# Kernel tuning notes

Measured on AMD Instinct MI355X. Metric: run time of the kernel, lower is better.

Reference implementation:

```python
import jax, jax.numpy as jnp
import numpy as np

N_NODES, N_LINKS, N_PATHS = 512, 4096, 20000
D = 128        # node_state_dim == path_state_dim
HEADS = 24
R = 256        # readout units
T_STEPS = 3    # config['t']
MAX_LEN = 8


def _gru(x, h, W, U, b):
    # Keras GRUCell (reset_after=True), gate order [z, r, h]
    xg = x @ W + b[0]
    hg = h @ U + b[1]
    xz, xr, xh = jnp.split(xg, 3, axis=-1)
    hz, hr, hh = jnp.split(hg, 3, axis=-1)
    z = jax.nn.sigmoid(xz + hz)
    r = jax.nn.sigmoid(xr + hr)
    hc = jnp.tanh(xh + r * hh)
    return z * h + (1.0 - z) * hc


def _masked_gru(x_seq, mask, h0, W, U, b, reverse):
    # x_seq [P,T,D], mask [P,T]; Keras masked RNN semantics:
    # state copies through masked steps, output copies previous output (init 0)
    if reverse:
        x_seq = x_seq[:, ::-1]
        mask = mask[:, ::-1]
    def step(carry, inp):
        h, o = carry
        x_t, m_t = inp
        h_new = _gru(x_t, h, W, U, b)
        m = m_t[:, None]
        h = jnp.where(m, h_new, h)
        o = jnp.where(m, h_new, o)
        return (h, o), o
    (hT, _), outs = jax.lax.scan(step, (h0, jnp.zeros_like(h0)),
                                 (x_seq.transpose(1, 0, 2), mask.T))
    outs = outs.transpose(1, 0, 2)
    if reverse:
        outs = outs[:, ::-1]
    return outs, hT


def _gat(x, adj, W, a_self, a_neigh, bias):
    # spektral-style dense GraphAttention, concat_heads=False (mean over heads)
    xp = jnp.einsum('nf,fhc->nhc', x, W)                 # [N,H,C]
    e_s = jnp.einsum('nhc,hc->nh', xp, a_self)
    e_n = jnp.einsum('nhc,hc->nh', xp, a_neigh)
    logits = e_s.T[:, :, None] + e_n.T[:, None, :]       # [H,N,N]
    logits = jax.nn.leaky_relu(logits, 0.2)
    logits = jnp.where(adj[None] == 0.0, -1e9, logits)
    attn = jax.nn.softmax(logits, axis=-1)
    return jnp.einsum('hij,jhc->ihc', attn, xp).mean(axis=1) + bias


def setup_inputs() -> dict:
    rng = np.random.default_rng(0)
    lens = rng.integers(4, MAX_LEN + 1, size=N_PATHS)
    paths = np.repeat(np.arange(N_PATHS, dtype=np.int32), lens)
    seqs = np.concatenate([np.arange(l, dtype=np.int32) for l in lens])
    nodes = rng.integers(0, N_NODES, size=paths.shape[0]).astype(np.int32)
    adj_idx = rng.choice(N_NODES * N_NODES, size=N_LINKS, replace=False).astype(np.int32)

    key = jax.random.key(0)
    ks = iter(jax.random.split(key, 40))
    nrm = lambda *s: jax.random.normal(next(ks), s, dtype=jnp.float32) * 0.05
    unif = lambda *s: jax.random.uniform(next(ks), s, dtype=jnp.float32)
    return {
        'ToS': unif(N_PATHS), 'bandwith': unif(N_PATHS),
        'q_policy': jnp.asarray(rng.integers(0, 3, N_NODES), jnp.float32),
        'w1': unif(N_NODES), 'w2': unif(N_NODES), 'w3': unif(N_NODES),
        'queue_size': unif(N_NODES, 3), 'link_capacity': unif(N_LINKS),
        'gat_W': nrm(D, HEADS, D), 'gat_as': nrm(HEADS, D), 'gat_an': nrm(HEADS, D),
        'gat_b': jnp.zeros((D,), jnp.float32),
        'Wp': nrm(D, 3 * D), 'Up': nrm(D, 3 * D), 'bp': jnp.zeros((2, 3 * D), jnp.float32),
        'Wb': nrm(D, 3 * D), 'Ub': nrm(D, 3 * D), 'bb': jnp.zeros((2, 3 * D), jnp.float32),
        'Wn': nrm(D, 3 * D), 'Un': nrm(D, 3 * D), 'bn': jnp.zeros((2, 3 * D), jnp.float32),
        'rW1': nrm(D, R), 'rb1': jnp.zeros((R,), jnp.float32),
        'rW2': nrm(R, R), 'rb2': jnp.zeros((R,), jnp.float32),
        'rW3': nrm(R, 1), 'rb3': jnp.zeros((1,), jnp.float32),
        'paths': jnp.asarray(paths), 'seqs': jnp.asarray(seqs),
        'nodes': jnp.asarray(nodes), 'adj_idx': jnp.asarray(adj_idx),
    }


def reference(ToS, bandwith, q_policy, w1, w2, w3, queue_size, link_capacity,
              gat_W, gat_as, gat_an, gat_b, Wp, Up, bp, Wb, Ub, bb, Wn, Un, bn,
              rW1, rb1, rW2, rb2, rW3, rb3, paths, seqs, nodes, adj_idx):
    node_state = jnp.concatenate([q_policy[:, None], w1[:, None], w2[:, None],
                                  w3[:, None], queue_size,
                                  jnp.zeros((N_NODES, D - 7), jnp.float32)], axis=1)
    path_state = jnp.concatenate([bandwith[:, None], ToS[:, None],
                                  jnp.zeros((N_PATHS, D - 2), jnp.float32)], axis=1)
    adj = jnp.zeros(N_NODES * N_NODES, jnp.float32).at[adj_idx].set(link_capacity)
    adj = adj.reshape(N_NODES, N_NODES)
    adj = adj / jnp.sqrt(jnp.sum(adj * adj))  # tf.linalg.normalize (global L2)

    lens = jax.ops.segment_sum(jnp.ones_like(paths), paths, num_segments=N_PATHS)
    mask = jnp.arange(MAX_LEN)[None, :] < lens[:, None]  # [P,T]

    for _ in range(T_STEPS):
        node_state = _gat(node_state, adj, gat_W, gat_as, gat_an, gat_b)
        h_tild = node_state[nodes]  # [S,D]
        node_inputs = jnp.zeros((N_PATHS, MAX_LEN, D), jnp.float32).at[paths, seqs].set(h_tild)
        out_f, h_f = _masked_gru(node_inputs, mask, path_state, Wp, Up, bp, False)
        out_b, _ = _masked_gru(node_inputs, mask, path_state, Wb, Ub, bb, True)
        outputs = out_f + out_b  # Bidirectional merge_mode='sum'
        path_state = h_f
        m2 = outputs[paths, seqs]
        m2 = jax.ops.segment_sum(m2, nodes, num_segments=N_NODES)
        node_state = _gru(m2, node_state, Wn, Un, bn)

    h = jax.nn.selu(path_state @ rW1 + rb1)
    h = jax.nn.relu(h @ rW2 + rb2)
    return h @ rW3 + rb3
```

## Files before the change

kernel.cpp:

```cpp
#include <hip/hip_runtime.h>
#include <math.h>

#define NN 512
#define NP 20000
#define DD 128
#define NH 24
#define G3 384
#define NHD 3072

typedef __attribute__((ext_vector_type(8))) short bf8_t;
typedef __attribute__((ext_vector_type(4))) float f4_t;
typedef unsigned short ushort_t;

__device__ __forceinline__ float sigf(float x){
  return __builtin_amdgcn_rcpf(1.f + __expf(-x));
}
__device__ __forceinline__ float tanh_fast(float x){
  float ax = fabsf(x);
  float e = __expf(-2.f*ax);
  float t = (1.f - e) * __builtin_amdgcn_rcpf(1.f + e);
  return copysignf(t, x);
}
__device__ __forceinline__ unsigned short f2bf(float f){
  unsigned int u = __float_as_uint(f);
  unsigned int r = (u + 0x7fffu + ((u>>16)&1u)) >> 16;
  return (unsigned short)r;
}
__device__ __forceinline__ float bf2f(unsigned short h){
  return __uint_as_float(((unsigned int)h)<<16);
}

__global__ void k_init_ns(float* ns, const float* qp, const float* w1, const float* w2,
                          const float* w3, const float* qs){
  int n = blockIdx.x, c = threadIdx.x;
  float v = 0.f;
  if (c==0) v=qp[n]; else if (c==1) v=w1[n]; else if (c==2) v=w2[n]; else if (c==3) v=w3[n];
  else if (c<7) v=qs[n*3 + (c-4)];
  ns[n*DD+c]=v;
}

__global__ void k_init_ps(float* ps, const float* bw, const float* tos){
  int i = blockIdx.x*256 + threadIdx.x;
  if (i >= NP*DD) return;
  int p = i>>7, c = i&127;
  float v=0.f; if(c==0) v=bw[p]; else if(c==1) v=tos[p];
  ps[i]=v;
}

__global__ void k_adj(unsigned int* adjb, const int* idx, const float* lc){
  int l = blockIdx.x*256+threadIdx.x; if(l>=4096) return;
  if (lc[l]!=0.f){
    int a = idx[l]; int i = a>>9, j = a&511;
    atomicOr(&adjb[i*16 + (j>>5)], 1u<<(j&31));
  }
}

__global__ void k_meta(const int* paths, const int* seqs, int* start, int* lens, int E){
  int e = blockIdx.x*256+threadIdx.x; if(e>=E) return;
  int p=paths[e], s=seqs[e];
  if (s==0) start[p]=e;
  if (e==E-1 || paths[e+1]!=p) lens[p]=s+1;
}

__global__ void k_lcount(const int* __restrict__ lens, int* lcnt){
  int p = blockIdx.x*256+threadIdx.x; if(p>=NP) return;
  atomicAdd(&lcnt[lens[p]],1);
}
__global__ void k_lscan(const int* __restrict__ lcnt, int* loff, int* lcur){
  if (threadIdx.x==0){
    int acc=0;
    for (int L=15; L>=0; --L){ loff[L]=acc; lcur[L]=acc; acc+=lcnt[L]; }
  }
}
__global__ void k_lfill(const int* __restrict__ lens, int* lcur, int* perm){
  int p = blockIdx.x*256+threadIdx.x; if(p>=NP) return;
  int pos = atomicAdd(&lcur[lens[p]],1);
  perm[pos]=p;
}

__global__ void k_wsplit(const float* __restrict__ W, ushort_t* __restrict__ Wh,
                         ushort_t* __restrict__ Wl, int shift, int ncols, int total){
  int i = blockIdx.x*256 + threadIdx.x;
  if (i >= total) return;
  int col = i >> shift, k = i & ((1<<shift)-1);
  float v = W[(size_t)k*ncols + col];
  ushort_t h = f2bf(v);
  Wh[i] = h; Wl[i] = f2bf(v - bf2f(h));
}

__global__ void k_wsplit6(
    const float* S0,const float* S1,const float* S2,const float* S3,const float* S4,const float* S5,
    ushort_t* H0, ushort_t* L0, ushort_t* H1, ushort_t* L1, ushort_t* H2, ushort_t* L2,
    ushort_t* H3, ushort_t* L3, ushort_t* H4, ushort_t* L4, ushort_t* H5, ushort_t* L5){
  int i = blockIdx.x*256 + threadIdx.x;
  if (i >= 6*G3*DD) return;
  int m = i/(G3*DD), r = i - m*(G3*DD);
  const float* S = m==0?S0:m==1?S1:m==2?S2:m==3?S3:m==4?S4:S5;
  ushort_t* Hh = m==0?H0:m==1?H1:m==2?H2:m==3?H3:m==4?H4:H5;
  ushort_t* Ll = m==0?L0:m==1?L1:m==2?L2:m==3?L3:m==4?L4:L5;
  int col = r>>7, k = r&127;
  float v = S[(size_t)k*G3 + col];
  ushort_t h = f2bf(v);
  Hh[r] = h; Ll[r] = f2bf(v - bf2f(h));
}

__global__ void k_gbw(const float* __restrict__ gb,
                      const float* __restrict__ Wp, const float* __restrict__ Wb,
                      const float* __restrict__ Un,
                      const float* __restrict__ bp, const float* __restrict__ bb,
                      float* bxgF, float* bxgB, float* gbUn){
  int m = blockIdx.x; int j = threadIdx.x;
  const float* W = m==0?Wp:(m==1?Wb:Un);
  float a = m==0?bp[j]:(m==1?bb[j]:0.f);
  for (int k=0;k<128;k++) a += gb[k]*W[(size_t)k*G3+j];
  (m==0?bxgF:(m==1?bxgB:gbUn))[j]=a;
}

__global__ __launch_bounds__(512) void k_xp2(const float* __restrict__ ns,
                      const ushort_t* __restrict__ gwh, const ushort_t* __restrict__ gwl,
                      const float* __restrict__ as_, const float* __restrict__ an_,
                      float* __restrict__ xp, float* __restrict__ es, float* __restrict__ en){
  __shared__ __align__(16) ushort_t XsH[32][136], XsL[32][136];
  __shared__ float ered[8][32][2];
  int r0 = blockIdx.x*32, c0 = blockIdx.y*256;
  int tid = threadIdx.x;
  int w = tid>>6, l = tid&63, lr = l&15, lg = l>>4;
  for (int idx=tid; idx<32*128; idx+=512){
    int pp=idx>>7, kk=idx&127;
    float v = ns[(size_t)(r0+pp)*DD+kk];
    ushort_t hi=f2bf(v); XsH[pp][kk]=hi; XsL[pp][kk]=f2bf(v-bf2f(hi));
  }
  __syncthreads();
  int col0 = c0 + w*32 + lr, col1 = col0 + 16;
  f4_t a00=(f4_t)(0.f), a01=(f4_t)(0.f), a10=(f4_t)(0.f), a11=(f4_t)(0.f);
  #pragma unroll
  for (int kt=0; kt<4; kt++){
    int kof = kt*32 + lg*8;
    const bf8_t Ah0 = *(const bf8_t*)&XsH[lr][kof];
    const bf8_t Al0 = *(const bf8_t*)&XsL[lr][kof];
    const bf8_t Ah1 = *(const bf8_t*)&XsH[16+lr][kof];
    const bf8_t Al1 = *(const bf8_t*)&XsL[16+lr][kof];
    const bf8_t B0h = *(const bf8_t*)(gwh + (size_t)col0*128 + kof);
    const bf8_t B0l = *(const bf8_t*)(gwl + (size_t)col0*128 + kof);
    const bf8_t B1h = *(const bf8_t*)(gwh + (size_t)col1*128 + kof);
    const bf8_t B1l = *(const bf8_t*)(gwl + (size_t)col1*128 + kof);
    a00 = __builtin_amdgcn_mfma_f32_16x16x32_bf16(Ah0,B0h,a00,0,0,0);
    a00 = __builtin_amdgcn_mfma_f32_16x16x32_bf16(Al0,B0h,a00,0,0,0);
    a00 = __builtin_amdgcn_mfma_f32_16x16x32_bf16(Ah0,B0l,a00,0,0,0);
    a01 = __builtin_amdgcn_mfma_f32_16x16x32_bf16(Ah0,B1h,a01,0,0,0);
    a01 = __builtin_amdgcn_mfma_f32_16x16x32_bf16(Al0,B1h,a01,0,0,0);
    a01 = __builtin_amdgcn_mfma_f32_16x16x32_bf16(Ah0,B1l,a01,0,0,0);
    a10 = __builtin_amdgcn_mfma_f32_16x16x32_bf16(Ah1,B0h,a10,0,0,0);
    a10 = __builtin_amdgcn_mfma_f32_16x16x32_bf16(Al1,B0h,a10,0,0,0);
    a10 = __builtin_amdgcn_mfma_f32_16x16x32_bf16(Ah1,B0l,a10,0,0,0);
    a11 = __builtin_amdgcn_mfma_f32_16x16x32_bf16(Ah1,B1h,a11,0,0,0);
    a11 = __builtin_amdgcn_mfma_f32_16x16x32_bf16(Al1,B1h,a11,0,0,0);
    a11 = __builtin_amdgcn_mfma_f32_16x16x32_bf16(Ah1,B1l,a11,0,0,0);
  }
  #pragma unroll
  for (int q=0;q<4;q++){
    int row0 = lg*4+q, row1 = 16+lg*4+q;
    xp[(size_t)(r0+row0)*NHD + col0] = a00[q];
    xp[(size_t)(r0+row0)*NHD + col1] = a01[q];
    xp[(size_t)(r0+row1)*NHD + col0] = a10[q];
    xp[(size_t)(r0+row1)*NHD + col1] = a11[q];
  }
  {
    int hw = blockIdx.y*2 + (w>>2);
    int cc0 = (w*32 + lr)&127, cc1 = (w*32 + 16 + lr)&127;
    float as0 = as_[hw*DD+cc0], as1 = as_[hw*DD+cc1];
    float an0 = an_[hw*DD+cc0], an1 = an_[hw*DD+cc1];
    #pragma unroll
    for (int q=0;q<4;q++){
      float s0 = a00[q]*as0 + a01[q]*as1;
      float n0 = a00[q]*an0 + a01[q]*an1;
      float s1 = a10[q]*as0 + a11[q]*as1;
      float n1 = a10[q]*an0 + a11[q]*an1;
      #pragma unroll
      for (int o=1;o<16;o<<=1){
        s0 += __shfl_xor(s0,o); n0 += __shfl_xor(n0,o);
        s1 += __shfl_xor(s1,o); n1 += __shfl_xor(n1,o);
      }
      if (lr==0){
        ered[w][lg*4+q][0]=s0;    ered[w][lg*4+q][1]=n0;
        ered[w][16+lg*4+q][0]=s1; ered[w][16+lg*4+q][1]=n1;
      }
    }
  }
  __syncthreads();
  if (tid < 128){
    int row = tid&31, hh = (tid>>5)&1, which = tid>>6;
    float v = ered[hh*4+0][row][which] + ered[hh*4+1][row][which]
            + ered[hh*4+2][row][which] + ered[hh*4+3][row][which];
    float* dst = which? en : es;
    dst[(size_t)(r0+row)*NH + blockIdx.y*2 + hh] = v;
  }
}

__global__ __launch_bounds__(256) void k_attn(const float* __restrict__ xp,
                      const float* __restrict__ es, const float* __restrict__ en,
                      const unsigned int* __restrict__ adjb, float* __restrict__ gout){
  __shared__ float lg[32][513];
  __shared__ float mxs[32], isms[32];
  int h = blockIdx.x, it = blockIdx.y; int i0 = it*32; int tid = threadIdx.x;
  for (int idx=tid; idx<32*512; idx+=256){
    int ii = idx>>9, j = idx&511;
    float l = es[(i0+ii)*NH+h] + en[j*NH+h];
    l = (l>=0.f)? l : 0.2f*l;
    unsigned int m = adjb[(i0+ii)*16 + (j>>5)];
    if (!((m>>(j&31))&1u)) l = -1000000000.0f;
    lg[ii][j] = l;
  }
  __syncthreads();
  {
    int t8 = tid&7, ii = tid>>3;
    float m = -INFINITY;
    for (int j=t8;j<512;j+=8) m = fmaxf(m, lg[ii][j]);
    for (int o=4;o>0;o>>=1) m = fmaxf(m, __shfl_xor(m, o));
    float s=0.f;
    for (int j=t8;j<512;j+=8) s += __expf(lg[ii][j]-m);
    for (int o=4;o>0;o>>=1) s += __shfl_xor(s,o);
    if (t8==0){ mxs[ii]=m; isms[ii]=__builtin_amdgcn_rcpf(s); }
  }
  __syncthreads();
  for (int idx=tid; idx<32*512; idx+=256){
    int ii = idx>>9, j = idx&511;
    lg[ii][j] = __expf(lg[ii][j]-mxs[ii])*isms[ii];
  }
  __syncthreads();
  int cq = tid&31, iq = tid>>5; int c = cq*4;
  float4 acc0=make_float4(0,0,0,0), acc1=acc0, acc2=acc0, acc3=acc0;
  for (int j=0;j<512;j++){
    const float4 xv = *(const float4*)(xp + ((size_t)j*NH + h)*DD + c);
    float p0 = lg[iq*4+0][j], p1 = lg[iq*4+1][j], p2 = lg[iq*4+2][j], p3 = lg[iq*4+3][j];
    acc0.x+=p0*xv.x; acc0.y+=p0*xv.y; acc0.z+=p0*xv.z; acc0.w+=p0*xv.w;
    acc1.x+=p1*xv.x; acc1.y+=p1*xv.y; acc1.z+=p1*xv.z; acc1.w+=p1*xv.w;
    acc2.x+=p2*xv.x; acc2.y+=p2*xv.y; acc2.z+=p2*xv.z; acc2.w+=p2*xv.w;
    acc3.x+=p3*xv.x; acc3.y+=p3*xv.y; acc3.z+=p3*xv.z; acc3.w+=p3*xv.w;
  }
  const float inv = 1.f/24.f;
  float* o0 = gout + (size_t)(i0+iq*4+0)*DD + c;
  float* o1 = gout + (size_t)(i0+iq*4+1)*DD + c;
  float* o2 = gout + (size_t)(i0+iq*4+2)*DD + c;
  float* o3 = gout + (size_t)(i0+iq*4+3)*DD + c;
  atomicAdd(o0+0,acc0.x*inv); atomicAdd(o0+1,acc0.y*inv); atomicAdd(o0+2,acc0.z*inv); atomicAdd(o0+3,acc0.w*inv);
  atomicAdd(o1+0,acc1.x*inv); atomicAdd(o1+1,acc1.y*inv); atomicAdd(o1+2,acc1.z*inv); atomicAdd(o1+3,acc1.w*inv);
  atomicAdd(o2+0,acc2.x*inv); atomicAdd(o2+1,acc2.y*inv); atomicAdd(o2+2,acc2.z*inv); atomicAdd(o2+3,acc2.w*inv);
  atomicAdd(o3+0,acc3.x*inv); atomicAdd(o3+1,acc3.y*inv); atomicAdd(o3+2,acc3.z*inv); atomicAdd(o3+3,acc3.w*inv);
}

__global__ __launch_bounds__(512) void k_xg3(const float* __restrict__ gout,
      const ushort_t* __restrict__ WpH, const ushort_t* __restrict__ WpL,
      const ushort_t* __restrict__ WbH, const ushort_t* __restrict__ WbL,
      const float* __restrict__ bxgF, const float* __restrict__ bxgB,
      float* __restrict__ xgF, float* __restrict__ xgB){
  __shared__ __align__(16) ushort_t XsH[32][136], XsL[32][136];
  int r0 = blockIdx.x*32;
  int mat = blockIdx.y/3, cg = blockIdx.y%3;
  const ushort_t* Wh = mat? WbH : WpH;
  const ushort_t* Wl = mat? WbL : WpL;
  const float* b0 = mat? bxgB : bxgF;
  float* out = mat? xgB : xgF;
  int tid = threadIdx.x;
  int w = tid>>6, l = tid&63, lr = l&15, lg = l>>4;
  for (int idx=tid; idx<32*128; idx+=512){
    int pp=idx>>7, kk=idx&127;
    float v = gout[(size_t)(r0+pp)*DD+kk];
    ushort_t hi=f2bf(v); XsH[pp][kk]=hi; XsL[pp][kk]=f2bf(v-bf2f(hi));
  }
  __syncthreads();
  int col = cg*128 + w*16 + lr;
  f4_t a0=(f4_t)(0.f), a1=(f4_t)(0.f);
  #pragma unroll
  for (int kt=0; kt<4; kt++){
    int kof = kt*32 + lg*8;
    const bf8_t Ah0 = *(const bf8_t*)&XsH[lr][kof];
    const bf8_t Al0 = *(const bf8_t*)&XsL[lr][kof];
    const bf8_t Ah1 = *(const bf8_t*)&XsH[16+lr][kof];
    const bf8_t Al1 = *(const bf8_t*)&XsL[16+lr][kof];
    const bf8_t Bh = *(const bf8_t*)(Wh + (size_t)col*128 + kof);
    const bf8_t Bl = *(const bf8_t*)(Wl + (size_t)col*128 + kof);
    a0 = __builtin_amdgcn_mfma_f32_16x16x32_bf16(Ah0,Bh,a0,0,0,0);
    a0 = __builtin_amdgcn_mfma_f32_16x16x32_bf16(Al0,Bh,a0,0,0,0);
    a0 = __builtin_amdgcn_mfma_f32_16x16x32_bf16(Ah0,Bl,a0,0,0,0);
    a1 = __builtin_amdgcn_mfma_f32_16x16x32_bf16(Ah1,Bh,a1,0,0,0);
    a1 = __builtin_amdgcn_mfma_f32_16x16x32_bf16(Al1,Bh,a1,0,0,0);
    a1 = __builtin_amdgcn_mfma_f32_16x16x32_bf16(Ah1,Bl,a1,0,0,0);
  }
  float bb0 = b0[col];
  #pragma unroll
  for (int q=0;q<4;q++){
    out[(size_t)(r0+lg*4+q)*G3 + col]    = a0[q] + bb0;
    out[(size_t)(r0+16+lg*4+q)*G3 + col] = a1[q] + bb0;
  }
}

__global__ __launch_bounds__(512) void k_gru2(
    const float* __restrict__ ps_in, float* __restrict__ ps_out,
    const float* __restrict__ xgF, const float* __restrict__ xgB,
    const ushort_t* __restrict__ UthF, const ushort_t* __restrict__ UtlF,
    const ushort_t* __restrict__ UthB, const ushort_t* __restrict__ UtlB,
    const float* __restrict__ b1F, const float* __restrict__ b1B,
    const int* __restrict__ start, const int* __restrict__ lens,
    const int* __restrict__ nodes, const int* __restrict__ perm,
    float* __restrict__ m2)
{
  __shared__ __align__(16) ushort_t HsH[2][32][136];
  __shared__ __align__(16) ushort_t HsL[2][32][136];
  __shared__ int Ls[32], Ss[32], Pid[32];
  __shared__ int nid_l[32][8];

  int dir = blockIdx.x & 1, pblk = blockIdx.x >> 1;
  const bool rev = (dir==1);
  const float* xg = rev ? xgB : xgF;
  const ushort_t* Uth = rev ? UthB : UthF;
  const ushort_t* Utl = rev ? UtlB : UtlF;
  const float* b1 = rev ? b1B : b1F;
  float* psn = rev ? (float*)0 : ps_out;

  int pb = pblk*32;
  int tid = threadIdx.x;
  int w = tid>>6, l = tid&63;
  int lr = l&15, lg = l>>4;
  int c = w*16 + lr;

  if (tid<32){ int pid = perm[pb+tid]; Pid[tid]=pid; Ls[tid]=lens[pid]; Ss[tid]=start[pid]; }
  __syncthreads();
  for (int idx=tid; idx<32*128; idx+=512){
    int pp=idx>>7, kk=idx&127;
    float v = ps_in[(size_t)Pid[pp]*DD+kk];
    ushort_t hi = f2bf(v);
    HsH[0][pp][kk]=hi; HsL[0][pp][kk]=f2bf(v - bf2f(hi));
  }
  if (tid<256){
    int p=tid>>3, s=tid&7; int L=Ls[p];
    int nid = 0;
    if (s<L){ int pos = rev ? (L-1-s) : s; nid = nodes[Ss[p]+pos]; }
    nid_l[p][s]=nid;
  }
  __syncthreads();

  int Lmax = Ls[0];
  int Lv[8];
  #pragma unroll
  for (int i=0;i<8;i++){ int p=(i>>2)*16 + lg*4 + (i&3); Lv[i]=Ls[p]; }
  float b1z = b1[c], b1r = b1[128+c], b1h = b1[256+c];

  int cur = 0;
  for (int s=0;s<Lmax;s++){
    int nxt = cur^1;
    bool act[8]; int niv[8]; float xzv[8], xrv[8], xhv[8];
    #pragma unroll
    for (int i=0;i<8;i++){
      int p=(i>>2)*16 + lg*4 + (i&3);
      act[i] = (s < Lv[i]);
      int nid = nid_l[p][s];
      niv[i] = nid;
      const float* xr = xg + (size_t)nid*G3;
      xzv[i]=xr[c]; xrv[i]=xr[128+c]; xhv[i]=xr[256+c];
    }
    f4_t accz0=(f4_t)(0.f), accz1=(f4_t)(0.f);
    f4_t accr0=(f4_t)(0.f), accr1=(f4_t)(0.f);
    f4_t acch0=(f4_t)(0.f), acch1=(f4_t)(0.f);
    #pragma unroll
    for (int kt=0; kt<4; kt++){
      int kof = kt*32 + lg*8;
      const bf8_t Ahi0 = *(const bf8_t*)&HsH[cur][lr][kof];
      const bf8_t Alo0 = *(const bf8_t*)&HsL[cur][lr][kof];
      const bf8_t Ahi1 = *(const bf8_t*)&HsH[cur][16+lr][kof];
      const bf8_t Alo1 = *(const bf8_t*)&HsL[cur][16+lr][kof];
      const bf8_t Bhz = *(const bf8_t*)(Uth + ((size_t)(      c))*128 + kof);
      const bf8_t Blz = *(const bf8_t*)(Utl + ((size_t)(      c))*128 + kof);
      const bf8_t Bhr = *(const bf8_t*)(Uth + ((size_t)(128 + c))*128 + kof);
      const bf8_t Blr = *(const bf8_t*)(Utl + ((size_t)(128 + c))*128 + kof);
      const bf8_t Bhh = *(const bf8_t*)(Uth + ((size_t)(256 + c))*128 + kof);
      const bf8_t Blh = *(const bf8_t*)(Utl + ((size_t)(256 + c))*128 + kof);
      accz0 = __builtin_amdgcn_mfma_f32_16x16x32_bf16(Ahi0, Bhz, accz0, 0,0,0);
      accz0 = __builtin_amdgcn_mfma_f32_16x16x32_bf16(Alo0, Bhz, accz0, 0,0,0);
      accz0 = __builtin_amdgcn_mfma_f32_16x16x32_bf16(Ahi0, Blz, accz0, 0,0,0);
      accz1 = __builtin_amdgcn_mfma_f32_16x16x32_bf16(Ahi1, Bhz, accz1, 0,0,0);
      accz1 = __builtin_amdgcn_mfma_f32_16x16x32_bf16(Alo1, Bhz, accz1, 0,0,0);
      accz1 = __builtin_amdgcn_mfma_f32_16x16x32_bf16(Ahi1, Blz, accz1, 0,0,0);
      accr0 = __builtin_amdgcn_mfma_f32_16x16x32_bf16(Ahi0, Bhr, accr0, 0,0,0);
      accr0 = __builtin_amdgcn_mfma_f32_16x16x32_bf16(Alo0, Bhr, accr0, 0,0,0);
      accr0 = __builtin_amdgcn_mfma_f32_16x16x32_bf16(Ahi0, Blr, accr0, 0,0,0);
      accr1 = __builtin_amdgcn_mfma_f32_16x16x32_bf16(Ahi1, Bhr, accr1, 0,0,0);
      accr1 = __builtin_amdgcn_mfma_f32_16x16x32_bf16(Alo1, Bhr, accr1, 0,0,0);
      accr1 = __builtin_amdgcn_mfma_f32_16x16x32_bf16(Ahi1, Blr, accr1, 0,0,0);
      acch0 = __builtin_amdgcn_mfma_f32_16x16x32_bf16(Ahi0, Bhh, acch0, 0,0,0);
      acch0 = __builtin_amdgcn_mfma_f32_16x16x32_bf16(Alo0, Bhh, acch0, 0,0,0);
      acch0 = __builtin_amdgcn_mfma_f32_16x16x32_bf16(Ahi0, Blh, acch0, 0,0,0);
      acch1 = __builtin_amdgcn_mfma_f32_16x16x32_bf16(Ahi1, Bhh, acch1, 0,0,0);
      acch1 = __builtin_amdgcn_mfma_f32_16x16x32_bf16(Alo1, Bhh, acch1, 0,0,0);
      acch1 = __builtin_amdgcn_mfma_f32_16x16x32_bf16(Ahi1, Blh, acch1, 0,0,0);
    }
#define EPI(i, mt, qq, AZ, AR, AH) { \
    int p = (mt)*16 + lg*4 + (qq); \
    if (act[i]) { \
      float hold = bf2f(HsH[cur][p][c]) + bf2f(HsL[cur][p][c]); \
      float z = sigf(xzv[i] + (AZ) + b1z); \
      float r = sigf(xrv[i] + (AR) + b1r); \
      float hc = tanh_fast(xhv[i] + r*((AH) + b1h)); \
      float hn = z*hold + (1.f-z)*hc; \
      ushort_t hi2 = f2bf(hn); \
      HsH[nxt][p][c]=hi2; HsL[nxt][p][c]=f2bf(hn - bf2f(hi2)); \
      atomicAdd(&m2[(size_t)niv[i]*DD + c], hn); \
    } else { \
      HsH[nxt][p][c]=HsH[cur][p][c]; HsL[nxt][p][c]=HsL[cur][p][c]; \
    } }
    EPI(0,0,0, accz0.x, accr0.x, acch0.x)
    EPI(1,0,1, accz0.y, accr0.y, acch0.y)
    EPI(2,0,2, accz0.z, accr0.z, acch0.z)
    EPI(3,0,3, accz0.w, accr0.w, acch0.w)
    EPI(4,1,0, accz1.x, accr1.x, acch1.x)
    EPI(5,1,1, accz1.y, accr1.y, acch1.y)
    EPI(6,1,2, accz1.z, accr1.z, acch1.z)
    EPI(7,1,3, accz1.w, accr1.w, acch1.w)
#undef EPI
    __syncthreads();
    cur = nxt;
  }
  if (psn){
    for (int idx=tid; idx<32*128; idx+=512){
      int pp=idx>>7, kk=idx&127;
      psn[(size_t)Pid[pp]*DD+kk] = bf2f(HsH[cur][pp][kk]) + bf2f(HsL[cur][pp][kk]);
    }
  }
}

__global__ __launch_bounds__(512) void k_ngru3(
    const float* __restrict__ m2, const float* __restrict__ gout,
    const ushort_t* __restrict__ WnH, const ushort_t* __restrict__ WnL,
    const ushort_t* __restrict__ UnH, const ushort_t* __restrict__ UnL,
    const float* __restrict__ bn, const float* __restrict__ gb,
    const float* __restrict__ gbUn, float* __restrict__ ns)
{
  __shared__ __align__(16) ushort_t MsH[32][136], MsL[32][136];
  __shared__ __align__(16) ushort_t GsH[32][136], GsL[32][136];
  int r0 = blockIdx.x*32;
  int tid = threadIdx.x;
  int w = tid>>6, l = tid&63, lr = l&15, lg = l>>4;
  for (int idx=tid; idx<32*128; idx+=512){
    int pp=idx>>7, kk=idx&127;
    float vm = m2[(size_t)(r0+pp)*DD+kk];
    float vg = gout[(size_t)(r0+pp)*DD+kk];
    ushort_t hm=f2bf(vm); MsH[pp][kk]=hm; MsL[pp][kk]=f2bf(vm-bf2f(hm));
    ushort_t hg=f2bf(vg); GsH[pp][kk]=hg; GsL[pp][kk]=f2bf(vg-bf2f(hg));
  }
  __syncthreads();
  int c = w*16 + lr;
  f4_t xz0=(f4_t)(0.f), xr0=(f4_t)(0.f), xh0=(f4_t)(0.f);
  f4_t xz1=(f4_t)(0.f), xr1=(f4_t)(0.f), xh1=(f4_t)(0.f);
  f4_t hz0=(f4_t)(0.f), hr0=(f4_t)(0.f), hh0=(f4_t)(0.f);
  f4_t hz1=(f4_t)(0.f), hr1=(f4_t)(0.f), hh1=(f4_t)(0.f);
  #pragma unroll
  for (int kt=0; kt<4; kt++){
    int kof = kt*32 + lg*8;
    const bf8_t MA0h = *(const bf8_t*)&MsH[lr][kof];
    const bf8_t MA0l = *(const bf8_t*)&MsL[lr][kof];
    const bf8_t MA1h = *(const bf8_t*)&MsH[16+lr][kof];
    const bf8_t MA1l = *(const bf8_t*)&MsL[16+lr][kof];
    const bf8_t GA0h = *(const bf8_t*)&GsH[lr][kof];
    const bf8_t GA0l = *(const bf8_t*)&GsL[lr][kof];
    const bf8_t GA1h = *(const bf8_t*)&GsH[16+lr][kof];
    const bf8_t GA1l = *(const bf8_t*)&GsL[16+lr][kof];
    const bf8_t Wzh = *(const bf8_t*)(WnH + ((size_t)(      c))*128 + kof);
    const bf8_t Wzl = *(const bf8_t*)(WnL + ((size_t)(      c))*128 + kof);
    const bf8_t Wrh = *(const bf8_t*)(WnH + ((size_t)(128 + c))*128 + kof);
    const bf8_t Wrl = *(const bf8_t*)(WnL + ((size_t)(128 + c))*128 + kof);
    const bf8_t Whh = *(const bf8_t*)(WnH + ((size_t)(256 + c))*128 + kof);
    const bf8_t Whl = *(const bf8_t*)(WnL + ((size_t)(256 + c))*128 + kof);
    const bf8_t Uzh = *(const bf8_t*)(UnH + ((size_t)(      c))*128 + kof);
    const bf8_t Uzl = *(const bf8_t*)(UnL + ((size_t)(      c))*128 + kof);
    const bf8_t Urh = *(const bf8_t*)(UnH + ((size_t)(128 + c))*128 + kof);
    const bf8_t Url = *(const bf8_t*)(UnL + ((size_t)(128 + c))*128 + kof);
    const bf8_t Uhh = *(const bf8_t*)(UnH + ((size_t)(256 + c))*128 + kof);
    const bf8_t Uhl = *(const bf8_t*)(UnL + ((size_t)(256 + c))*128 + kof);
    xz0 = __builtin_amdgcn_mfma_f32_16x16x32_bf16(MA0h,Wzh,xz0,0,0,0);
    xz0 = __builtin_amdgcn_mfma_f32_16x16x32_bf16(MA0l,Wzh,xz0,0,0,0);
    xz0 = __builtin_amdgcn_mfma_f32_16x16x32_bf16(MA0h,Wzl,xz0,0,0,0);
    xz1 = __builtin_amdgcn_mfma_f32_16x16x32_bf16(MA1h,Wzh,xz1,0,0,0);
    xz1 = __builtin_amdgcn_mfma_f32_16x16x32_bf16(MA1l,Wzh,xz1,0,0,0);
    xz1 = __builtin_amdgcn_mfma_f32_16x16x32_bf16(MA1h,Wzl,xz1,0,0,0);
    xr0 = __builtin_amdgcn_mfma_f32_16x16x32_bf16(MA0h,Wrh,xr0,0,0,0);
    xr0 = __builtin_amdgcn_mfma_f32_16x16x32_bf16(MA0l,Wrh,xr0,0,0,0);
    xr0 = __builtin_amdgcn_mfma_f32_16x16x32_bf16(MA0h,Wrl,xr0,0,0,0);
    xr1 = __builtin_amdgcn_mfma_f32_16x16x32_bf16(MA1h,Wrh,xr1,0,0,0);
    xr1 = __builtin_amdgcn_mfma_f32_16x16x32_bf16(MA1l,Wrh,xr1,0,0,0);
    xr1 = __builtin_amdgcn_mfma_f32_16x16x32_bf16(MA1h,Wrl,xr1,0,0,0);
    xh0 = __builtin_amdgcn_mfma_f32_16x16x32_bf16(MA0h,Whh,xh0,0,0,0);
    xh0 = __builtin_amdgcn_mfma_f32_16x16x32_bf16(MA0l,Whh,xh0,0,0,0);
    xh0 = __builtin_amdgcn_mfma_f32_16x16x32_bf16(MA0h,Whl,xh0,0,0,0);
    xh1 = __builtin_amdgcn_mfma_f32_16x16x32_bf16(MA1h,Whh,xh1,0,0,0);
    xh1 = __builtin_amdgcn_mfma_f32_16x16x32_bf16(MA1l,Whh,xh1,0,0,0);
    xh1 = __builtin_amdgcn_mfma_f32_16x16x32_bf16(MA1h,Whl,xh1,0,0,0);
    hz0 = __builtin_amdgcn_mfma_f32_16x16x32_bf16(GA0h,Uzh,hz0,0,0,0);
    hz0 = __builtin_amdgcn_mfma_f32_16x16x32_bf16(GA0l,Uzh,hz0,0,0,0);
    hz0 = __builtin_amdgcn_mfma_f32_16x16x32_bf16(GA0h,Uzl,hz0,0,0,0);
    hz1 = __builtin_amdgcn_mfma_f32_16x16x32_bf16(GA1h,Uzh,hz1,0,0,0);
    hz1 = __builtin_amdgcn_mfma_f32_16x16x32_bf16(GA1l,Uzh,hz1,0,0,0);
    hz1 = __builtin_amdgcn_mfma_f32_16x16x32_bf16(GA1h,Uzl,hz1,0,0,0);
    hr0 = __builtin_amdgcn_mfma_f32_16x16x32_bf16(GA0h,Urh,hr0,0,0,0);
    hr0 = __builtin_amdgcn_mfma_f32_16x16x32_bf16(GA0l,Urh,hr0,0,0,0);
    hr0 = __builtin_amdgcn_mfma_f32_16x16x32_bf16(GA0h,Url,hr0,0,0,0);
    hr1 = __builtin_amdgcn_mfma_f32_16x16x32_bf16(GA1h,Urh,hr1,0,0,0);
    hr1 = __builtin_amdgcn_mfma_f32_16x16x32_bf16(GA1l,Urh,hr1,0,0,0);
    hr1 = __builtin_amdgcn_mfma_f32_16x16x32_bf16(GA1h,Url,hr1,0,0,0);
    hh0 = __builtin_amdgcn_mfma_f32_16x16x32_bf16(GA0h,Uhh,hh0,0,0,0);
    hh0 = __builtin_amdgcn_mfma_f32_16x16x32_bf16(GA0l,Uhh,hh0,0,0,0);
    hh0 = __builtin_amdgcn_mfma_f32_16x16x32_bf16(GA0h,Uhl,hh0,0,0,0);
    hh1 = __builtin_amdgcn_mfma_f32_16x16x32_bf16(GA1h,Uhh,hh1,0,0,0);
    hh1 = __builtin_amdgcn_mfma_f32_16x16x32_bf16(GA1l,Uhh,hh1,0,0,0);
    hh1 = __builtin_amdgcn_mfma_f32_16x16x32_bf16(GA1h,Uhl,hh1,0,0,0);
  }
  float bz = bn[c] + bn[G3+c] + gbUn[c];
  float br = bn[128+c] + bn[G3+128+c] + gbUn[128+c];
  float bxh = bn[256+c], bhh = bn[G3+256+c] + gbUn[256+c];
  float gbc = gb[c];
  #pragma unroll
  for (int q=0;q<4;q++){
    {
      int n = lg*4+q;
      float hval = bf2f(GsH[n][c]) + bf2f(GsL[n][c]) + gbc;
      float z = sigf(xz0[q] + hz0[q] + bz);
      float r = sigf(xr0[q] + hr0[q] + br);
      float hc = tanh_fast(xh0[q] + bxh + r*(hh0[q] + bhh));
      ns[(size_t)(r0+n)*DD + c] = z*hval + (1.f-z)*hc;
    }
    {
      int n = 16+lg*4+q;
      float hval = bf2f(GsH[n][c]) + bf2f(GsL[n][c]) + gbc;
      float z = sigf(xz1[q] + hz1[q] + bz);
      float r = sigf(xr1[q] + hr1[q] + br);
      float hc = tanh_fast(xh1[q] + bxh + r*(hh1[q] + bhh));
      ns[(size_t)(r0+n)*DD + c] = z*hval + (1.f-z)*hc;
    }
  }
}

__global__ __launch_bounds__(512) void k_read2(
    const float* __restrict__ ps,
    const ushort_t* __restrict__ r1h, const ushort_t* __restrict__ r1l,
    const ushort_t* __restrict__ r2h, const ushort_t* __restrict__ r2l,
    const float* __restrict__ rb1, const float* __restrict__ rb2,
    const float* __restrict__ rW3, const float* __restrict__ rb3,
    float* __restrict__ out)
{
  __shared__ __align__(16) ushort_t XsH[32][136], XsL[32][136];
  __shared__ __align__(16) char buf[32*264*2*2];
  ushort_t (*H1H)[264] = (ushort_t(*)[264])buf;
  ushort_t (*H1L)[264] = (ushort_t(*)[264])(buf + 32*264*2);
  float (*H2)[257] = (float(*)[257])buf;
  int pb = blockIdx.x*32, tid = threadIdx.x;
  int w = tid>>6, l = tid&63, lr = l&15, lg = l>>4;
  for (int idx=tid; idx<32*128; idx+=512){
    int pp=idx>>7, kk=idx&127;
    float v = ps[(size_t)(pb+pp)*DD+kk];
    ushort_t hi=f2bf(v); XsH[pp][kk]=hi; XsL[pp][kk]=f2bf(v-bf2f(hi));
  }
  __syncthreads();
  int col0 = w*32 + lr, col1 = col0 + 16;
  f4_t a00=(f4_t)(0.f), a01=(f4_t)(0.f), a10=(f4_t)(0.f), a11=(f4_t)(0.f);
  #pragma unroll
  for (int kt=0; kt<4; kt++){
    int kof = kt*32 + lg*8;
    const bf8_t Ah0 = *(const bf8_t*)&XsH[lr][kof];
    const bf8_t Al0 = *(const bf8_t*)&XsL[lr][kof];
    const bf8_t Ah1 = *(const bf8_t*)&XsH[16+lr][kof];
    const bf8_t Al1 = *(const bf8_t*)&XsL[16+lr][kof];
    const bf8_t B0h = *(const bf8_t*)(r1h + (size_t)col0*128 + kof);
    const bf8_t B0l = *(const bf8_t*)(r1l + (size_t)col0*128 + kof);
    const bf8_t B1h = *(const bf8_t*)(r1h + (size_t)col1*128 + kof);
    const bf8_t B1l = *(const bf8_t*)(r1l + (size_t)col1*128 + kof);
    a00 = __builtin_amdgcn_mfma_f32_16x16x32_bf16(Ah0,B0h,a00,0,0,0);
    a00 = __builtin_amdgcn_mfma_f32_16x16x32_bf16(Al0,B0h,a00,0,0,0);
    a00 = __builtin_amdgcn_mfma_f32_16x16x32_bf16(Ah0,B0l,a00,0,0,0);
    a01 = __builtin_amdgcn_mfma_f32_16x16x32_bf16(Ah0,B1h,a01,0,0,0);
    a01 = __builtin_amdgcn_mfma_f32_16x16x32_bf16(Al0,B1h,a01,0,0,0);
    a01 = __builtin_amdgcn_mfma_f32_16x16x32_bf16(Ah0,B1l,a01,0,0,0);
    a10 = __builtin_amdgcn_mfma_f32_16x16x32_bf16(Ah1,B0h,a10,0,0,0);
    a10 = __builtin_amdgcn_mfma_f32_16x16x32_bf16(Al1,B0h,a10,0,0,0);
    a10 = __builtin_amdgcn_mfma_f32_16x16x32_bf16(Ah1,B0l,a10,0,0,0);
    a11 = __builtin_amdgcn_mfma_f32_16x16x32_bf16(Ah1,B1h,a11,0,0,0);
    a11 = __builtin_amdgcn_mfma_f32_16x16x32_bf16(Al1,B1h,a11,0,0,0);
    a11 = __builtin_amdgcn_mfma_f32_16x16x32_bf16(Ah1,B1l,a11,0,0,0);
  }
  float rb1c0 = rb1[col0], rb1c1 = rb1[col1];
  #pragma unroll
  for (int q=0;q<4;q++){
    int row0 = lg*4+q, row1 = 16+lg*4+q;
    float v00 = a00[q]+rb1c0, v01 = a01[q]+rb1c1, v10 = a10[q]+rb1c0, v11 = a11[q]+rb1c1;
    v00 = 1.0507009873554805f * (v00>0.f ? v00 : 1.6732632423543772f*(__expf(v00)-1.f));
    v01 = 1.0507009873554805f * (v01>0.f ? v01 : 1.6732632423543772f*(__expf(v01)-1.f));
    v10 = 1.0507009873554805f * (v10>0.f ? v10 : 1.6732632423543772f*(__expf(v10)-1.f));
    v11 = 1.0507009873554805f * (v11>0.f ? v11 : 1.6732632423543772f*(__expf(v11)-1.f));
    ushort_t h;
    h=f2bf(v00); H1H[row0][col0]=h; H1L[row0][col0]=f2bf(v00-bf2f(h));
    h=f2bf(v01); H1H[row0][col1]=h; H1L[row0][col1]=f2bf(v01-bf2f(h));
    h=f2bf(v10); H1H[row1][col0]=h; H1L[row1][col0]=f2bf(v10-bf2f(h));
    h=f2bf(v11); H1H[row1][col1]=h; H1L[row1][col1]=f2bf(v11-bf2f(h));
  }
  __syncthreads();
  f4_t c00=(f4_t)(0.f), c01=(f4_t)(0.f), c10=(f4_t)(0.f), c11=(f4_t)(0.f);
  #pragma unroll
  for (int kt=0; kt<8; kt++){
    int kof = kt*32 + lg*8;
    const bf8_t Ah0 = *(const bf8_t*)&H1H[lr][kof];
    const bf8_t Al0 = *(const bf8_t*)&H1L[lr][kof];
    const bf8_t Ah1 = *(const bf8_t*)&H1H[16+lr][kof];
    const bf8_t Al1 = *(const bf8_t*)&H1L[16+lr][kof];
    const bf8_t B0h = *(const bf8_t*)(r2h + (size_t)col0*256 + kof);
    const bf8_t B0l = *(const bf8_t*)(r2l + (size_t)col0*256 + kof);
    const bf8_t B1h = *(const bf8_t*)(r2h + (size_t)col1*256 + kof);
    const bf8_t B1l = *(const bf8_t*)(r2l + (size_t)col1*256 + kof);
    c00 = __builtin_amdgcn_mfma_f32_16x16x32_bf16(Ah0,B0h,c00,0,0,0);
    c00 = __builtin_amdgcn_mfma_f32_16x16x32_bf16(Al0,B0h,c00,0,0,0);
    c00 = __builtin_amdgcn_mfma_f32_16x16x32_bf16(Ah0,B0l,c00,0,0,0);
    c01 = __builtin_amdgcn_mfma_f32_16x16x32_bf16(Ah0,B1h,c01,0,0,0);
    c01 = __builtin_amdgcn_mfma_f32_16x16x32_bf16(Al0,B1h,c01,0,0,0);
    c01 = __builtin_amdgcn_mfma_f32_16x16x32_bf16(Ah0,B1l,c01,0,0,0);
    c10 = __builtin_amdgcn_mfma_f32_16x16x32_bf16(Ah1,B0h,c10,0,0,0);
    c10 = __builtin_amdgcn_mfma_f32_16x16x32_bf16(Al1,B0h,c10,0,0,0);
    c10 = __builtin_amdgcn_mfma_f32_16x16x32_bf16(Ah1,B0l,c10,0,0,0);
    c11 = __builtin_amdgcn_mfma_f32_16x16x32_bf16(Ah1,B1h,c11,0,0,0);
    c11 = __builtin_amdgcn_mfma_f32_16x16x32_bf16(Al1,B1h,c11,0,0,0);
    c11 = __builtin_amdgcn_mfma_f32_16x16x32_bf16(Ah1,B1l,c11,0,0,0);
  }
  __syncthreads();
  float rb2c0 = rb2[col0], rb2c1 = rb2[col1];
  #pragma unroll
  for (int q=0;q<4;q++){
    int row0 = lg*4+q, row1 = 16+lg*4+q;
    H2[row0][col0] = fmaxf(c00[q]+rb2c0, 0.f);
    H2[row0][col1] = fmaxf(c01[q]+rb2c1, 0.f);
    H2[row1][col0] = fmaxf(c10[q]+rb2c0, 0.f);
    H2[row1][col1] = fmaxf(c11[q]+rb2c1, 0.f);
  }
  __syncthreads();
  int r = tid>>4, j0 = tid&15;
  float s = 0.f;
  for (int j=j0; j<256; j+=16) s += H2[r][j]*rW3[j];
  for (int o=8;o>0;o>>=1) s += __shfl_xor(s,o);
  if (j0==0) out[pb+r] = s + rb3[0];
}

extern "C" void kernel_launch(void* const* d_in, const int* in_sizes, int n_in,
                              void* d_out, int out_size, void* d_ws, size_t ws_size,
                              hipStream_t stream)
{
  const float* ToS   = (const float*)d_in[0];
  const float* bw    = (const float*)d_in[1];
  const float* qpol  = (const float*)d_in[2];
  const float* w1    = (const float*)d_in[3];
  const float* w2    = (const float*)d_in[4];
  const float* w3    = (const float*)d_in[5];
  const float* qs    = (const float*)d_in[6];
  const float* lc    = (const float*)d_in[7];
  const float* gat_W = (const float*)d_in[8];
  const float* gat_as= (const float*)d_in[9];
  const float* gat_an= (const float*)d_in[10];
  const float* gat_b = (const float*)d_in[11];
  const float* Wp    = (const float*)d_in[12];
  const float* Up    = (const float*)d_in[13];
  const float* bp    = (const float*)d_in[14];
  const float* Wb    = (const float*)d_in[15];
  const float* Ub    = (const float*)d_in[16];
  const float* bb    = (const float*)d_in[17];
  const float* Wn    = (const float*)d_in[18];
  const float* Un    = (const float*)d_in[19];
  const float* bn    = (const float*)d_in[20];
  const float* rW1   = (const float*)d_in[21];
  const float* rb1   = (const float*)d_in[22];
  const float* rW2   = (const float*)d_in[23];
  const float* rb2   = (const float*)d_in[24];
  const float* rW3   = (const float*)d_in[25];
  const float* rb3   = (const float*)d_in[26];
  const int* paths   = (const int*)d_in[27];
  const int* seqs    = (const int*)d_in[28];
  const int* nodes   = (const int*)d_in[29];
  const int* adj_idx = (const int*)d_in[30];
  int E = in_sizes[27];

  char* w0 = (char*)d_ws;
  char* w = w0;
  auto alloc = [&](size_t nbytes)->void*{ void* r=(void*)w; w += (nbytes + 255) & ~(size_t)255; return r; };
  float* ns     = (float*)alloc((size_t)NN*DD*4);
  float* gout   = (float*)alloc((size_t)NN*DD*4);
  float* psA    = (float*)alloc((size_t)NP*DD*4);
  float* psB    = (float*)alloc((size_t)NP*DD*4);
  float* xp     = (float*)alloc((size_t)NN*NHD*4);
  float* es     = (float*)alloc((size_t)NN*NH*4);
  float* en     = (float*)alloc((size_t)NN*NH*4);
  unsigned int* adjb = (unsigned int*)alloc((size_t)NN*16*4);
  float* xgp    = (float*)alloc((size_t)NN*G3*4);
  float* xgb    = (float*)alloc((size_t)NN*G3*4);
  float* m2     = (float*)alloc((size_t)NN*DD*4);
  float* bxgF   = (float*)alloc((size_t)G3*4);
  float* bxgB   = (float*)alloc((size_t)G3*4);
  float* gbUn   = (float*)alloc((size_t)G3*4);
  ushort_t* Uthp = (ushort_t*)alloc((size_t)G3*DD*2);
  ushort_t* Utlp = (ushort_t*)alloc((size_t)G3*DD*2);
  ushort_t* Uthb = (ushort_t*)alloc((size_t)G3*DD*2);
  ushort_t* Utlb = (ushort_t*)alloc((size_t)G3*DD*2);
  ushort_t* Wpth = (ushort_t*)alloc((size_t)G3*DD*2);
  ushort_t* Wptl = (ushort_t*)alloc((size_t)G3*DD*2);
  ushort_t* Wbth = (ushort_t*)alloc((size_t)G3*DD*2);
  ushort_t* Wbtl = (ushort_t*)alloc((size_t)G3*DD*2);
  ushort_t* WnTh = (ushort_t*)alloc((size_t)G3*DD*2);
  ushort_t* WnTl = (ushort_t*)alloc((size_t)G3*DD*2);
  ushort_t* UnTh = (ushort_t*)alloc((size_t)G3*DD*2);
  ushort_t* UnTl = (ushort_t*)alloc((size_t)G3*DD*2);
  ushort_t* r1h = (ushort_t*)alloc((size_t)256*128*2);
  ushort_t* r1l = (ushort_t*)alloc((size_t)256*128*2);
  ushort_t* r2h = (ushort_t*)alloc((size_t)256*256*2);
  ushort_t* r2l = (ushort_t*)alloc((size_t)256*256*2);
  ushort_t* gwh = (ushort_t*)alloc((size_t)NHD*DD*2);
  ushort_t* gwl = (ushort_t*)alloc((size_t)NHD*DD*2);
  int* start    = (int*)alloc((size_t)NP*4);
  int* lens     = (int*)alloc((size_t)NP*4);
  int* perm     = (int*)alloc((size_t)NP*4);
  int* lcnt     = (int*)alloc(16*4);
  int* loff     = (int*)alloc(16*4);
  int* lcur     = (int*)alloc(16*4);
  (void)n_in; (void)out_size; (void)ws_size;

  hipMemsetAsync(adjb, 0, (size_t)NN*16*4, stream);
  hipMemsetAsync(lcnt, 0, 16*4, stream);
  k_init_ns<<<NN,DD,0,stream>>>(ns, qpol, w1, w2, w3, qs);
  k_init_ps<<<(NP*DD+255)/256,256,0,stream>>>(psA, bw, ToS);
  k_adj<<<16,256,0,stream>>>(adjb, adj_idx, lc);
  k_meta<<<(E+255)/256,256,0,stream>>>(paths, seqs, start, lens, E);
  k_lcount<<<(NP+255)/256,256,0,stream>>>(lens, lcnt);
  k_lscan<<<1,64,0,stream>>>(lcnt, loff, lcur);
  k_lfill<<<(NP+255)/256,256,0,stream>>>(lens, lcur, perm);
  k_wsplit6<<<(6*G3*DD+255)/256,256,0,stream>>>(Up, Ub, Wp, Wb, Wn, Un,
      Uthp,Utlp, Uthb,Utlb, Wpth,Wptl, Wbth,Wbtl, WnTh,WnTl, UnTh,UnTl);
  k_wsplit<<<(256*128+255)/256,256,0,stream>>>(rW1, r1h, r1l, 7, 256, 256*128);
  k_wsplit<<<(256*256+255)/256,256,0,stream>>>(rW2, r2h, r2l, 8, 256, 256*256);
  k_wsplit<<<(NHD*DD+255)/256,256,0,stream>>>(gat_W, gwh, gwl, 7, NHD, NHD*DD);
  k_gbw<<<3,G3,0,stream>>>(gat_b, Wp, Wb, Un, bp, bb, bxgF, bxgB, gbUn);

  float* ps_cur = psA; float* ps_nxt = psB;
  for (int t=0;t<3;t++){
    hipMemsetAsync(gout, 0, (size_t)NN*DD*4, stream);
    k_xp2<<<dim3(NN/32, NHD/256),512,0,stream>>>(ns, gwh, gwl, gat_as, gat_an, xp, es, en);
    k_attn<<<dim3(NH, NN/32),256,0,stream>>>(xp, es, en, adjb, gout);
    k_xg3<<<dim3(NN/32,6),512,0,stream>>>(gout, Wpth, Wptl, Wbth, Wbtl, bxgF, bxgB, xgp, xgb);
    hipMemsetAsync(m2, 0, (size_t)NN*DD*4, stream);
    k_gru2<<<2*(NP/32),512,0,stream>>>(ps_cur, ps_nxt, xgp, xgb, Uthp, Utlp, Uthb, Utlb,
                                       bp+G3, bb+G3, start, lens, nodes, perm, m2);
    k_ngru3<<<NN/32,512,0,stream>>>(m2, gout, WnTh, WnTl, UnTh, UnTl, bn, gat_b, gbUn, ns);
    float* tmp = ps_cur; ps_cur = ps_nxt; ps_nxt = tmp;
  }
  k_read2<<<NP/32,512,0,stream>>>(ps_cur, r1h, r1l, r2h, r2l, rb1, rb2, rW3, rb3, (float*)d_out);
}
```

Before: 1.239 ms.

## Compute GAT attention aggregation with split-bf16 MFMA over transposed projected features

The GAT projection kernel now writes its output transposed and split into bf16 high/low halves, so the attention kernel can run the attention-times-features product on MFMA with three-pass split-bf16 precision instead of scalar FP32 FMAs. The attention kernel also computes the softmax statistics in one online pass from cached logits inputs, removing the large FP32 logits buffer in shared memory. Costs are extra conversion work, some precision loss from the split-bf16 approximation, and still one atomic add per output element.

```diff
diff --git a/kernel.cpp b/kernel.cpp
--- a/kernel.cpp
+++ b/kernel.cpp
@@ -119,7 +119,8 @@
 __global__ __launch_bounds__(512) void k_xp2(const float* __restrict__ ns,
                       const ushort_t* __restrict__ gwh, const ushort_t* __restrict__ gwl,
                       const float* __restrict__ as_, const float* __restrict__ an_,
-                      float* __restrict__ xp, float* __restrict__ es, float* __restrict__ en){
+                      ushort_t* __restrict__ xpTh, ushort_t* __restrict__ xpTl,
+                      float* __restrict__ es, float* __restrict__ en){
   __shared__ __align__(16) ushort_t XsH[32][136], XsL[32][136];
   __shared__ float ered[8][32][2];
   int r0 = blockIdx.x*32, c0 = blockIdx.y*256;
@@ -157,13 +158,22 @@
     a11 = __builtin_amdgcn_mfma_f32_16x16x32_bf16(Al1,B1h,a11,0,0,0);
     a11 = __builtin_amdgcn_mfma_f32_16x16x32_bf16(Ah1,B1l,a11,0,0,0);
   }
-  #pragma unroll
-  for (int q=0;q<4;q++){
-    int row0 = lg*4+q, row1 = 16+lg*4+q;
-    xp[(size_t)(r0+row0)*NHD + col0] = a00[q];
-    xp[(size_t)(r0+row0)*NHD + col1] = a01[q];
-    xp[(size_t)(r0+row1)*NHD + col0] = a10[q];
-    xp[(size_t)(r0+row1)*NHD + col1] = a11[q];
+  {
+    ushort4 h00,l00,h01,l01,h10,l10,h11,l11;
+    #pragma unroll
+    for (int q=0;q<4;q++){
+      float v; ushort_t hh;
+      v=a00[q]; hh=f2bf(v); ((ushort_t*)&h00)[q]=hh; ((ushort_t*)&l00)[q]=f2bf(v-bf2f(hh));
+      v=a01[q]; hh=f2bf(v); ((ushort_t*)&h01)[q]=hh; ((ushort_t*)&l01)[q]=f2bf(v-bf2f(hh));
+      v=a10[q]; hh=f2bf(v); ((ushort_t*)&h10)[q]=hh; ((ushort_t*)&l10)[q]=f2bf(v-bf2f(hh));
+      v=a11[q]; hh=f2bf(v); ((ushort_t*)&h11)[q]=hh; ((ushort_t*)&l11)[q]=f2bf(v-bf2f(hh));
+    }
+    size_t b0 = (size_t)col0*NN + r0 + lg*4;
+    size_t b1 = (size_t)col1*NN + r0 + lg*4;
+    *(ushort4*)(xpTh + b0)      = h00; *(ushort4*)(xpTl + b0)      = l00;
+    *(ushort4*)(xpTh + b1)      = h01; *(ushort4*)(xpTl + b1)      = l01;
+    *(ushort4*)(xpTh + b0 + 16) = h10; *(ushort4*)(xpTl + b0 + 16) = l10;
+    *(ushort4*)(xpTh + b1 + 16) = h11; *(ushort4*)(xpTl + b1 + 16) = l11;
   }
   {
     int hw = blockIdx.y*2 + (w>>2);
@@ -197,56 +207,89 @@
   }
 }
 
-__global__ __launch_bounds__(256) void k_attn(const float* __restrict__ xp,
-                      const float* __restrict__ es, const float* __restrict__ en,
-                      const unsigned int* __restrict__ adjb, float* __restrict__ gout){
-  __shared__ float lg[32][513];
+__global__ __launch_bounds__(256) void k_attn2(
+    const ushort_t* __restrict__ xpTh, const ushort_t* __restrict__ xpTl,
+    const float* __restrict__ es, const float* __restrict__ en,
+    const unsigned int* __restrict__ adjb, float* __restrict__ gout)
+{
+  __shared__ __align__(16) ushort_t PsH[32][520], PsL[32][520];
+  __shared__ float enl[512], esl[32];
+  __shared__ unsigned int am[32][16];
   __shared__ float mxs[32], isms[32];
-  int h = blockIdx.x, it = blockIdx.y; int i0 = it*32; int tid = threadIdx.x;
+  int h = blockIdx.x, i0 = blockIdx.y*32, tid = threadIdx.x;
+  for (int j=tid; j<512; j+=256) enl[j] = en[(size_t)j*NH + h];
+  for (int idx=tid; idx<512; idx+=256) am[idx>>4][idx&15] = adjb[(i0+(idx>>4))*16 + (idx&15)];
+  if (tid<32) esl[tid] = es[(size_t)(i0+tid)*NH + h];
+  __syncthreads();
+  {
+    int t8 = tid&7, ii = tid>>3;
+    float esr = esl[ii];
+    float m = -INFINITY, s = 0.f;
+    for (int j=t8; j<512; j+=8){
+      float lv = esr + enl[j];
+      lv = (lv>=0.f)? lv : 0.2f*lv;
+      if (!((am[ii][j>>5]>>(j&31))&1u)) lv = -1000000000.0f;
+      if (lv > m){ s = s*__expf(m-lv) + 1.f; m = lv; }
+      else        s += __expf(lv-m);
+    }
+    #pragma unroll
+    for (int o=4;o>0;o>>=1){
+      float mo = __shfl_xor(m,o), so = __shfl_xor(s,o);
+      if (mo > m){ s = s*__expf(m-mo) + so; m = mo; }
+      else        s += so*__expf(mo-m);
+    }
+    if (t8==0){ mxs[ii]=m; isms[ii]=__builtin_amdgcn_rcpf(s); }
+  }
+  __syncthreads();
   for (int idx=tid; idx<32*512; idx+=256){
     int ii = idx>>9, j = idx&511;
-    float l = es[(i0+ii)*NH+h] + en[j*NH+h];
-    l = (l>=0.f)? l : 0.2f*l;
-    unsigned int m = adjb[(i0+ii)*16 + (j>>5)];
-    if (!((m>>(j&31))&1u)) l = -1000000000.0f;
-    lg[ii][j] = l;
-  }
-  __syncthreads();
-  {
-    int t8 = tid&7, ii = tid>>3;
-    float m = -INFINITY;
-    for (int j=t8;j<512;j+=8) m = fmaxf(m, lg[ii][j]);
-    for (int o=4;o>0;o>>=1) m = fmaxf(m, __shfl_xor(m, o));
-    float s=0.f;
-    for (int j=t8;j<512;j+=8) s += __expf(lg[ii][j]-m);
-    for (int o=4;o>0;o>>=1) s += __shfl_xor(s,o);
-    if (t8==0){ mxs[ii]=m; isms[ii]=__builtin_amdgcn_rcpf(s); }
-  }
-  __syncthreads();
-  for (int idx=tid; idx<32*512; idx+=256){
-    int ii = idx>>9, j = idx&511;
-    lg[ii][j] = __expf(lg[ii][j]-mxs[ii])*isms[ii];
-  }
-  __syncthreads();
-  int cq = tid&31, iq = tid>>5; int c = cq*4;
-  float4 acc0=make_float4(0,0,0,0), acc1=acc0, acc2=acc0, acc3=acc0;
-  for (int j=0;j<512;j++){
-    const float4 xv = *(const float4*)(xp + ((size_t)j*NH + h)*DD + c);
-    float p0 = lg[iq*4+0][j], p1 = lg[iq*4+1][j], p2 = lg[iq*4+2][j], p3 = lg[iq*4+3][j];
-    acc0.x+=p0*xv.x; acc0.y+=p0*xv.y; acc0.z+=p0*xv.z; acc0.w+=p0*xv.w;
-    acc1.x+=p1*xv.x; acc1.y+=p1*xv.y; acc1.z+=p1*xv.z; acc1.w+=p1*xv.w;
-    acc2.x+=p2*xv.x; acc2.y+=p2*xv.y; acc2.z+=p2*xv.z; acc2.w+=p2*xv.w;
-    acc3.x+=p3*xv.x; acc3.y+=p3*xv.y; acc3.z+=p3*xv.z; acc3.w+=p3*xv.w;
+    float lv = esl[ii] + enl[j];
+    lv = (lv>=0.f)? lv : 0.2f*lv;
+    if (!((am[ii][j>>5]>>(j&31))&1u)) lv = -1000000000.0f;
+    float p = __expf(lv - mxs[ii]) * isms[ii];
+    ushort_t hi = f2bf(p);
+    PsH[ii][j] = hi; PsL[ii][j] = f2bf(p - bf2f(hi));
+  }
+  __syncthreads();
+  int wv = tid>>6, ln = tid&63, lr = ln&15, lg = ln>>4;
+  const ushort_t* B0hp = xpTh + ((size_t)(h*DD + wv*32 + lr))*NN;
+  const ushort_t* B0lp = xpTl + ((size_t)(h*DD + wv*32 + lr))*NN;
+  const ushort_t* B1hp = B0hp + (size_t)16*NN;
+  const ushort_t* B1lp = B0lp + (size_t)16*NN;
+  f4_t a00=(f4_t)(0.f), a01=(f4_t)(0.f), a10=(f4_t)(0.f), a11=(f4_t)(0.f);
+  #pragma unroll
+  for (int kt=0; kt<16; kt++){
+    int kof = kt*32 + lg*8;
+    const bf8_t A0h = *(const bf8_t*)&PsH[lr][kof];
+    const bf8_t A0l = *(const bf8_t*)&PsL[lr][kof];
+    const bf8_t A1h = *(const bf8_t*)&PsH[16+lr][kof];
+    const bf8_t A1l = *(const bf8_t*)&PsL[16+lr][kof];
+    const bf8_t B0h = *(const bf8_t*)(B0hp + kof);
+    const bf8_t B0l = *(const bf8_t*)(B0lp + kof);
+    const bf8_t B1h = *(const bf8_t*)(B1hp + kof);
+    const bf8_t B1l = *(const bf8_t*)(B1lp + kof);
+    a00 = __builtin_amdgcn_mfma_f32_16x16x32_bf16(A0h,B0h,a00,0,0,0);
+    a00 = __builtin_amdgcn_mfma_f32_16x16x32_bf16(A0l,B0h,a00,0,0,0);
+    a00 = __builtin_amdgcn_mfma_f32_16x16x32_bf16(A0h,B0l,a00,0,0,0);
+    a01 = __builtin_amdgcn_mfma_f32_16x16x32_bf16(A0h,B1h,a01,0,0,0);
+    a01 = __builtin_amdgcn_mfma_f32_16x16x32_bf16(A0l,B1h,a01,0,0,0);
+    a01 = __builtin_amdgcn_mfma_f32_16x16x32_bf16(A0h,B1l,a01,0,0,0);
+    a10 = __builtin_amdgcn_mfma_f32_16x16x32_bf16(A1h,B0h,a10,0,0,0);
+    a10 = __builtin_amdgcn_mfma_f32_16x16x32_bf16(A1l,B0h,a10,0,0,0);
+    a10 = __builtin_amdgcn_mfma_f32_16x16x32_bf16(A1h,B0l,a10,0,0,0);
+    a11 = __builtin_amdgcn_mfma_f32_16x16x32_bf16(A1h,B1h,a11,0,0,0);
+    a11 = __builtin_amdgcn_mfma_f32_16x16x32_bf16(A1l,B1h,a11,0,0,0);
+    a11 = __builtin_amdgcn_mfma_f32_16x16x32_bf16(A1h,B1l,a11,0,0,0);
   }
   const float inv = 1.f/24.f;
-  float* o0 = gout + (size_t)(i0+iq*4+0)*DD + c;
-  float* o1 = gout + (size_t)(i0+iq*4+1)*DD + c;
-  float* o2 = gout + (size_t)(i0+iq*4+2)*DD + c;
-  float* o3 = gout + (size_t)(i0+iq*4+3)*DD + c;
-  atomicAdd(o0+0,acc0.x*inv); atomicAdd(o0+1,acc0.y*inv); atomicAdd(o0+2,acc0.z*inv); atomicAdd(o0+3,acc0.w*inv);
-  atomicAdd(o1+0,acc1.x*inv); atomicAdd(o1+1,acc1.y*inv); atomicAdd(o1+2,acc1.z*inv); atomicAdd(o1+3,acc1.w*inv);
-  atomicAdd(o2+0,acc2.x*inv); atomicAdd(o2+1,acc2.y*inv); atomicAdd(o2+2,acc2.z*inv); atomicAdd(o2+3,acc2.w*inv);
-  atomicAdd(o3+0,acc3.x*inv); atomicAdd(o3+1,acc3.y*inv); atomicAdd(o3+2,acc3.z*inv); atomicAdd(o3+3,acc3.w*inv);
+  #pragma unroll
+  for (int q=0;q<4;q++){
+    int r0w = lg*4+q, r1w = 16+lg*4+q;
+    atomicAdd(&gout[(size_t)(i0+r0w)*DD + wv*32 + lr],      a00[q]*inv);
+    atomicAdd(&gout[(size_t)(i0+r0w)*DD + wv*32 + 16 + lr], a01[q]*inv);
+    atomicAdd(&gout[(size_t)(i0+r1w)*DD + wv*32 + lr],      a10[q]*inv);
+    atomicAdd(&gout[(size_t)(i0+r1w)*DD + wv*32 + 16 + lr], a11[q]*inv);
+  }
 }
 
 __global__ __launch_bounds__(512) void k_xg3(const float* __restrict__ gout,
@@ -688,7 +731,8 @@
   float* gout   = (float*)alloc((size_t)NN*DD*4);
   float* psA    = (float*)alloc((size_t)NP*DD*4);
   float* psB    = (float*)alloc((size_t)NP*DD*4);
-  float* xp     = (float*)alloc((size_t)NN*NHD*4);
+  ushort_t* xpTh= (ushort_t*)alloc((size_t)NHD*NN*2);
+  ushort_t* xpTl= (ushort_t*)alloc((size_t)NHD*NN*2);
   float* es     = (float*)alloc((size_t)NN*NH*4);
   float* en     = (float*)alloc((size_t)NN*NH*4);
   unsigned int* adjb = (unsigned int*)alloc((size_t)NN*16*4);
@@ -743,8 +787,8 @@
   float* ps_cur = psA; float* ps_nxt = psB;
   for (int t=0;t<3;t++){
     hipMemsetAsync(gout, 0, (size_t)NN*DD*4, stream);
-    k_xp2<<<dim3(NN/32, NHD/256),512,0,stream>>>(ns, gwh, gwl, gat_as, gat_an, xp, es, en);
-    k_attn<<<dim3(NH, NN/32),256,0,stream>>>(xp, es, en, adjb, gout);
+    k_xp2<<<dim3(NN/32, NHD/256),512,0,stream>>>(ns, gwh, gwl, gat_as, gat_an, xpTh, xpTl, es, en);
+    k_attn2<<<dim3(NH, NN/32),256,0,stream>>>(xpTh, xpTl, es, en, adjb, gout);
     k_xg3<<<dim3(NN/32,6),512,0,stream>>>(gout, Wpth, Wptl, Wbth, Wbtl, bxgF, bxgB, xgp, xgb);
     hipMemsetAsync(m2, 0, (size_t)NN*DD*4, stream);
     k_gru2<<<2*(NP/32),512,0,stream>>>(ps_cur, ps_nxt, xgp, xgb, Uthp, Utlp, Uthb, Utlb,
```

Result: faster. 1.074 ms (-13.3%).
